# Performance work log

Measured on AMD Instinct MI355X. Metric: run time of the kernel, lower is better.

## Reference

```python
import jax, jax.numpy as jnp
import numpy as np

EMBED_DIM = 1024
NUM_HEADS = 16
HEAD_DIM = EMBED_DIM // NUM_HEADS
HIDDEN_DIM = int(EMBED_DIM * 4.0)
LN_EPS = 1e-5


def layer_norm(x, g, b):
    mu = jnp.mean(x, axis=-1, keepdims=True)
    var = jnp.var(x, axis=-1, keepdims=True)
    return (x - mu) * jax.lax.rsqrt(var + LN_EPS) * g + b


def setup_inputs() -> dict:
    key = jax.random.key(0)
    ks = jax.random.split(key, 8)
    D, H3, Dh = EMBED_DIM, 3 * EMBED_DIM, HIDDEN_DIM
    s = lambda fan: 1.0 / np.sqrt(fan)
    return {
        "x": jax.random.normal(ks[0], (2, 2048, D), dtype=jnp.float32),
        "ln1_g": jnp.ones((D,), jnp.float32),
        "ln1_b": jnp.zeros((D,), jnp.float32),
        "ln2_g": jnp.ones((D,), jnp.float32),
        "ln2_b": jnp.zeros((D,), jnp.float32),
        "w_qkv": jax.random.normal(ks[1], (D, H3), jnp.float32) * s(D),
        "b_qkv": jnp.zeros((H3,), jnp.float32),
        "w_proj": jax.random.normal(ks[2], (D, D), jnp.float32) * s(D),
        "b_proj": jnp.zeros((D,), jnp.float32),
        "w_fc1": jax.random.normal(ks[3], (D, Dh), jnp.float32) * s(D),
        "b_fc1": jnp.zeros((Dh,), jnp.float32),
        "w_fc2": jax.random.normal(ks[4], (Dh, D), jnp.float32) * s(Dh),
        "b_fc2": jnp.zeros((D,), jnp.float32),
    }


def reference(x, ln1_g, ln1_b, ln2_g, ln2_b, w_qkv, b_qkv, w_proj, b_proj,
              w_fc1, b_fc1, w_fc2, b_fc2):
    B, N, D = x.shape
    H, hd = NUM_HEADS, HEAD_DIM

    # --- attention branch (dropout inactive at eval) ---
    h = layer_norm(x, ln1_g, ln1_b)
    qkv = h @ w_qkv + b_qkv                      # [B,N,3D]
    qkv = qkv.reshape(B, N, 3, H, hd)
    q = qkv[:, :, 0].transpose(0, 2, 1, 3)       # [B,H,N,hd]
    k = qkv[:, :, 1].transpose(0, 2, 1, 3)
    v = qkv[:, :, 2].transpose(0, 2, 1, 3)
    scores = jnp.einsum('bhqd,bhkd->bhqk', q, k) / jnp.sqrt(jnp.float32(hd))
    attn = jax.nn.softmax(scores, axis=-1)
    ctx = jnp.einsum('bhqk,bhkd->bhqd', attn, v) # [B,H,N,hd]
    ctx = ctx.transpose(0, 2, 1, 3).reshape(B, N, D)
    x = x + ctx @ w_proj + b_proj

    # --- MLP branch ---
    h2 = layer_norm(x, ln2_g, ln2_b)
    h2 = jax.nn.gelu(h2 @ w_fc1 + b_fc1, approximate=False)  # torch nn.GELU = exact erf
    x = x + h2 @ w_fc2 + b_fc2
    return x
```

## Files before the change

### kernel.cpp

```cpp
#include <hip/hip_runtime.h>
#include <hip/hip_bf16.h>
#include <cstdint>

typedef __attribute__((ext_vector_type(8))) short short8;
typedef __attribute__((ext_vector_type(4))) float f32x4;

__device__ __forceinline__ uint16_t f2b(float f) {
  uint32_t u = __builtin_bit_cast(uint32_t, f);
  return (uint16_t)((u + 0x7FFFu + ((u >> 16) & 1u)) >> 16);
}
__device__ __forceinline__ float b2f(uint16_t h) {
  uint32_t u = ((uint32_t)h) << 16;
  return __builtin_bit_cast(float, u);
}
__device__ __forceinline__ void async16(void* lds, const void* g) {
  __builtin_amdgcn_global_load_lds(
      (const __attribute__((address_space(1))) uint32_t*)g,
      (__attribute__((address_space(3))) uint32_t*)lds, 16, 0, 0);
}
__device__ __forceinline__ void xcd_remap(int& bx, int& by, int& bz) {
  int gx = gridDim.x, gy = gridDim.y;
  int nwg = gx * gy * gridDim.z;
  int hw = blockIdx.x + gx * (blockIdx.y + gy * blockIdx.z);
  int work = ((nwg & 7) == 0) ? ((hw & 7) * (nwg >> 3) + (hw >> 3)) : hw;
  bx = work % gx;
  int t = work / gx;
  by = t % gy;
  bz = t / gy;
}

__global__ __launch_bounds__(256) void k_transpose_all(
    const float* __restrict__ wq, const float* __restrict__ wp,
    const float* __restrict__ w1, const float* __restrict__ w2,
    uint16_t* __restrict__ tq, uint16_t* __restrict__ tp,
    uint16_t* __restrict__ t1, uint16_t* __restrict__ t2) {
  __shared__ float tile[64][65];
  int id = blockIdx.x;
  const float* w; uint16_t* wT; int K, N, bx, by;
  if (id < 768)        { w = wq; wT = tq; K = 1024; N = 3072; bx = id % 48; by = id / 48; }
  else if (id < 1024)  { id -= 768;  w = wp; wT = tp; K = 1024; N = 1024; bx = id & 15; by = id >> 4; }
  else if (id < 2048)  { id -= 1024; w = w1; wT = t1; K = 1024; N = 4096; bx = id & 63; by = id >> 6; }
  else                 { id -= 2048; w = w2; wT = t2; K = 4096; N = 1024; bx = id & 15; by = id >> 4; }
  const int tx = threadIdx.x;
  const int k0 = by * 64, n0 = bx * 64;
  const int cr = tx & 15, rbase = tx >> 4;
#pragma unroll
  for (int rr = 0; rr < 4; ++rr) {
    int k = rbase + rr * 16;
    int n = cr * 4;
    float4 v = *(const float4*)&w[(size_t)(k0 + k) * N + (n0 + n)];
    tile[k][n + 0] = v.x; tile[k][n + 1] = v.y;
    tile[k][n + 2] = v.z; tile[k][n + 3] = v.w;
  }
  __syncthreads();
#pragma unroll
  for (int rr = 0; rr < 4; ++rr) {
    int n = rbase + rr * 16;
    int k = cr * 4;
    ushort4 o;
    o.x = f2b(tile[k + 0][n]);
    o.y = f2b(tile[k + 1][n]);
    o.z = f2b(tile[k + 2][n]);
    o.w = f2b(tile[k + 3][n]);
    *(ushort4*)&wT[(size_t)(n0 + n) * K + (k0 + k)] = o;
  }
}

__global__ __launch_bounds__(256) void k_layernorm(
    const float* __restrict__ x, const float* __restrict__ g,
    const float* __restrict__ b, uint16_t* __restrict__ out) {
  const int row = blockIdx.x * 4 + (threadIdx.x >> 6);
  const int lane = threadIdx.x & 63;
  const float* xr = x + (size_t)row * 1024;
  float4 v[4];
  float s = 0.f, ss = 0.f;
#pragma unroll
  for (int i = 0; i < 4; ++i) {
    v[i] = *(const float4*)&xr[i * 256 + lane * 4];
    s += v[i].x + v[i].y + v[i].z + v[i].w;
    ss += v[i].x * v[i].x + v[i].y * v[i].y + v[i].z * v[i].z + v[i].w * v[i].w;
  }
#pragma unroll
  for (int off = 1; off < 64; off <<= 1) {
    s += __shfl_xor(s, off);
    ss += __shfl_xor(ss, off);
  }
  float mu = s * (1.f / 1024.f);
  float rstd = rsqrtf(ss * (1.f / 1024.f) - mu * mu + 1e-5f);
#pragma unroll
  for (int i = 0; i < 4; ++i) {
    int col = i * 256 + lane * 4;
    float4 gv = *(const float4*)&g[col];
    float4 bv = *(const float4*)&b[col];
    ushort4 o;
    o.x = f2b((v[i].x - mu) * rstd * gv.x + bv.x);
    o.y = f2b((v[i].y - mu) * rstd * gv.y + bv.y);
    o.z = f2b((v[i].z - mu) * rstd * gv.z + bv.z);
    o.w = f2b((v[i].w - mu) * rstd * gv.w + bv.w);
    *(ushort4*)&out[(size_t)row * 1024 + col] = o;
  }
}

__global__ __launch_bounds__(256) void k_ln2_fuse(
    const float* __restrict__ x, const uint16_t* __restrict__ pp0,
    const uint16_t* __restrict__ pp1, const float* __restrict__ bias,
    const float* __restrict__ g, const float* __restrict__ b,
    float* __restrict__ x2, uint16_t* __restrict__ out) {
  const int row = blockIdx.x * 4 + (threadIdx.x >> 6);
  const int lane = threadIdx.x & 63;
  const size_t rb = (size_t)row * 1024;
  float4 v[4];
  float s = 0.f, ss = 0.f;
#pragma unroll
  for (int i = 0; i < 4; ++i) {
    int col = i * 256 + lane * 4;
    float4 xv = *(const float4*)&x[rb + col];
    float4 bv = *(const float4*)&bias[col];
    ushort4 a0 = *(const ushort4*)&pp0[rb + col];
    ushort4 a1 = *(const ushort4*)&pp1[rb + col];
    v[i].x = xv.x + bv.x + b2f(a0.x) + b2f(a1.x);
    v[i].y = xv.y + bv.y + b2f(a0.y) + b2f(a1.y);
    v[i].z = xv.z + bv.z + b2f(a0.z) + b2f(a1.z);
    v[i].w = xv.w + bv.w + b2f(a0.w) + b2f(a1.w);
    *(float4*)&x2[rb + col] = v[i];
    s += v[i].x + v[i].y + v[i].z + v[i].w;
    ss += v[i].x * v[i].x + v[i].y * v[i].y + v[i].z * v[i].z + v[i].w * v[i].w;
  }
#pragma unroll
  for (int off = 1; off < 64; off <<= 1) {
    s += __shfl_xor(s, off);
    ss += __shfl_xor(ss, off);
  }
  float mu = s * (1.f / 1024.f);
  float rstd = rsqrtf(ss * (1.f / 1024.f) - mu * mu + 1e-5f);
#pragma unroll
  for (int i = 0; i < 4; ++i) {
    int col = i * 256 + lane * 4;
    float4 gv = *(const float4*)&g[col];
    float4 bv = *(const float4*)&b[col];
    ushort4 o;
    o.x = f2b((v[i].x - mu) * rstd * gv.x + bv.x);
    o.y = f2b((v[i].y - mu) * rstd * gv.y + bv.y);
    o.z = f2b((v[i].z - mu) * rstd * gv.z + bv.z);
    o.w = f2b((v[i].w - mu) * rstd * gv.w + bv.w);
    *(ushort4*)&out[rb + col] = o;
  }
}

__global__ __launch_bounds__(256) void k_fc2_reduce(
    const float* __restrict__ x2, const uint16_t* __restrict__ f0,
    const uint16_t* __restrict__ f1, const float* __restrict__ bias,
    float* __restrict__ out, int N) {
  int i = (blockIdx.x * 256 + threadIdx.x) * 4;
  float4 v = *(const float4*)&x2[i];
  float4 bv = *(const float4*)&bias[i & (N - 1)];
  ushort4 a0 = *(const ushort4*)&f0[i];
  ushort4 a1 = *(const ushort4*)&f1[i];
  v.x += bv.x + b2f(a0.x) + b2f(a1.x);
  v.y += bv.y + b2f(a0.y) + b2f(a1.y);
  v.z += bv.z + b2f(a0.z) + b2f(a1.z);
  v.w += bv.w + b2f(a0.w) + b2f(a1.w);
  *(float4*)&out[i] = v;
}

template <int EPI>
__global__ __launch_bounds__(256) void k_gemm(
    const uint16_t* __restrict__ A, const uint16_t* __restrict__ Bt,
    const float* __restrict__ bias, void* __restrict__ Cout,
    uint16_t* __restrict__ vTout, int M, int N, int K) {
  __shared__ __align__(16) uint16_t Alds[128 * 64];
  __shared__ __align__(16) uint16_t Blds[128 * 64];
  int bx, by, bz;
  xcd_remap(bx, by, bz);
  const int tid = threadIdx.x;
  const int lane = tid & 63;
  const int w = tid >> 6;
  const int wr = w >> 1, wc = w & 1;
  const int m0 = by * 128, n0 = bx * 128;
  const int l15 = lane & 15, l4 = lane >> 4;
  const uint16_t* pA[4];
  const uint16_t* pB[4];
#pragma unroll
  for (int c = 0; c < 4; ++c) {
    int i = c * 256 + tid;
    int row = i >> 3, d = (i & 7) * 8;
    pA[c] = A + (size_t)(m0 + row) * K + d;
    pB[c] = Bt + (size_t)(n0 + row) * K + d;
  }
  f32x4 acc[4][4] = {};
  for (int k0 = 0; k0 < K; k0 += 64) {
#pragma unroll
    for (int c = 0; c < 4; ++c) {
      async16(&Alds[(c * 256 + tid) * 8], pA[c]);
      pA[c] += 64;
    }
#pragma unroll
    for (int c = 0; c < 4; ++c) {
      async16(&Blds[(c * 256 + tid) * 8], pB[c]);
      pB[c] += 64;
    }
    __syncthreads();
#pragma unroll
    for (int kc = 0; kc < 2; ++kc) {
      short8 af[4], bf[4];
#pragma unroll
      for (int m = 0; m < 4; ++m)
        af[m] = *(const short8*)&Alds[(wr * 64 + m * 16 + l15) * 64 + kc * 32 + l4 * 8];
#pragma unroll
      for (int n = 0; n < 4; ++n)
        bf[n] = *(const short8*)&Blds[(wc * 64 + n * 16 + l15) * 64 + kc * 32 + l4 * 8];
#pragma unroll
      for (int m = 0; m < 4; ++m)
#pragma unroll
        for (int n = 0; n < 4; ++n)
          acc[m][n] = __builtin_amdgcn_mfma_f32_16x16x32_bf16(af[m], bf[n], acc[m][n], 0, 0, 0);
    }
    __syncthreads();
  }
#pragma unroll
  for (int m = 0; m < 4; ++m) {
#pragma unroll
    for (int n = 0; n < 4; ++n) {
      int col = n0 + wc * 64 + n * 16 + l15;
      int rowb = m0 + wr * 64 + m * 16 + l4 * 4;
      float bv = bias[col];
      if constexpr (EPI == 3) {
        if (col >= 2048) {
          int dtot = col - 2048;
          int hh = dtot >> 6, dd = dtot & 63;
          int bg = rowb >> 11, tl = rowb & 2047;
          ushort4 ov;
          ov.x = f2b(acc[m][n][0] + bv);
          ov.y = f2b(acc[m][n][1] + bv);
          ov.z = f2b(acc[m][n][2] + bv);
          ov.w = f2b(acc[m][n][3] + bv);
          *(ushort4*)&vTout[(((size_t)(bg * 16 + hh)) * 64 + dd) * 2048 + tl] = ov;
          continue;
        }
      }
#pragma unroll
      for (int r = 0; r < 4; ++r) {
        float val = acc[m][n][r] + bv;
        size_t idx = (size_t)(rowb + r) * N + col;
        if constexpr (EPI == 2) {
          float u = val * val;
          float a = fmaf(u, 0.1029480545f, 2.3022078158f);
          float t = exp2f(val * a);
          float gl = val - val / (t + 1.0f);
          ((uint16_t*)Cout)[idx] = f2b(gl);
        } else {
          ((uint16_t*)Cout)[idx] = f2b(val);
        }
      }
    }
  }
}

__global__ __launch_bounds__(256) void k_gemm_splitk(
    const uint16_t* __restrict__ A, const uint16_t* __restrict__ Bt,
    uint16_t* __restrict__ p0, uint16_t* __restrict__ p1,
    int M, int N, int K, int Kc) {
  __shared__ __align__(16) uint16_t Alds[128 * 64];
  __shared__ __align__(16) uint16_t Blds[128 * 64];
  int bx, by, bz;
  xcd_remap(bx, by, bz);
  const int tid = threadIdx.x;
  const int lane = tid & 63;
  const int w = tid >> 6;
  const int wr = w >> 1, wc = w & 1;
  const int m0 = by * 128, n0 = bx * 128;
  const int l15 = lane & 15, l4 = lane >> 4;
  const int kbeg = bz * Kc;
  uint16_t* __restrict__ P = (bz == 0) ? p0 : p1;
  const uint16_t* pA[4];
  const uint16_t* pB[4];
#pragma unroll
  for (int c = 0; c < 4; ++c) {
    int i = c * 256 + tid;
    int row = i >> 3, d = (i & 7) * 8;
    pA[c] = A + (size_t)(m0 + row) * K + kbeg + d;
    pB[c] = Bt + (size_t)(n0 + row) * K + kbeg + d;
  }
  f32x4 acc[4][4] = {};
  for (int k0 = 0; k0 < Kc; k0 += 64) {
#pragma unroll
    for (int c = 0; c < 4; ++c) {
      async16(&Alds[(c * 256 + tid) * 8], pA[c]);
      pA[c] += 64;
    }
#pragma unroll
    for (int c = 0; c < 4; ++c) {
      async16(&Blds[(c * 256 + tid) * 8], pB[c]);
      pB[c] += 64;
    }
    __syncthreads();
#pragma unroll
    for (int kc = 0; kc < 2; ++kc) {
      short8 af[4], bf[4];
#pragma unroll
      for (int m = 0; m < 4; ++m)
        af[m] = *(const short8*)&Alds[(wr * 64 + m * 16 + l15) * 64 + kc * 32 + l4 * 8];
#pragma unroll
      for (int n = 0; n < 4; ++n)
        bf[n] = *(const short8*)&Blds[(wc * 64 + n * 16 + l15) * 64 + kc * 32 + l4 * 8];
#pragma unroll
      for (int m = 0; m < 4; ++m)
#pragma unroll
        for (int n = 0; n < 4; ++n)
          acc[m][n] = __builtin_amdgcn_mfma_f32_16x16x32_bf16(af[m], bf[n], acc[m][n], 0, 0, 0);
    }
    __syncthreads();
  }
#pragma unroll
  for (int m = 0; m < 4; ++m) {
#pragma unroll
    for (int n = 0; n < 4; ++n) {
      int col = n0 + wc * 64 + n * 16 + l15;
      int rowb = m0 + wr * 64 + m * 16 + l4 * 4;
#pragma unroll
      for (int r = 0; r < 4; ++r)
        P[(size_t)(rowb + r) * N + col] = f2b(acc[m][n][r]);
    }
  }
}

__global__ __launch_bounds__(256, 4) void k_attn(
    const uint16_t* __restrict__ qkv, const uint16_t* __restrict__ vT,
    uint16_t* __restrict__ ctx) {
  __shared__ __align__(16) uint16_t Klds[2][64 * 64];
  __shared__ __align__(16) uint16_t Vlds[2][64 * 64];
  __shared__ __align__(16) uint16_t Plds[4][16 * 64];
  int bx, by, bz;
  xcd_remap(bx, by, bz);
  const int bh = by, qt = bx;
  const int b = bh >> 4, h = bh & 15;
  const int tid = threadIdx.x, lane = tid & 63, w = tid >> 6;
  const int l15 = lane & 15, l4 = lane >> 4;
  const int sw = (l15 & 7) << 3;
  const size_t tokbase = (size_t)b * 2048;

  const float QSC = 0.125f * 1.44269504088896340736f;
  short8 qa[2];
  const int qrow = qt * 64 + w * 16 + l15;
#pragma unroll
  for (int kc = 0; kc < 2; ++kc) {
    short8 v = *(const short8*)&qkv[(tokbase + qrow) * 3072 + h * 64 + kc * 32 + l4 * 8];
#pragma unroll
    for (int j = 0; j < 8; ++j) v[j] = (short)f2b(b2f((uint16_t)v[j]) * QSC);
    qa[kc] = v;
  }
  short8 ones;
#pragma unroll
  for (int j = 0; j < 8; ++j) ones[j] = (short)0x3F80;

  float m_s = -1e30f;
  f32x4 o[4] = {};
  f32x4 ol = {};

  const uint16_t* pK[2];
  const uint16_t* pV[2];
#pragma unroll
  for (int c = 0; c < 2; ++c) {
    int i = c * 256 + tid;
    int row = i >> 3, colE = (i & 7) * 8;
    int colS = colE ^ ((row & 7) << 3);
    pK[c] = qkv + (tokbase + row) * 3072 + 1024 + h * 64 + colS;
    int tkS = colE ^ ((row & 7) << 3);
    pV[c] = vT + ((size_t)bh * 64 + row) * 2048 + tkS;
  }

  auto stage = [&](int buf) {
#pragma unroll
    for (int c = 0; c < 2; ++c) {
      async16(&Klds[buf][(c * 256 + tid) * 8], pK[c]);
      pK[c] += 64 * 3072;
    }
#pragma unroll
    for (int c = 0; c < 2; ++c) {
      async16(&Vlds[buf][(c * 256 + tid) * 8], pV[c]);
      pV[c] += 64;
    }
  };

  stage(0);
  __syncthreads();
  int cur = 0;

  for (int t0 = 0; t0 < 2048; t0 += 64) {
    if (t0 + 64 < 2048) stage(cur ^ 1);

    f32x4 s[4] = {};
    __builtin_amdgcn_s_setprio(1);
#pragma unroll
    for (int kc = 0; kc < 2; ++kc) {
      const int cc = (kc * 32 + l4 * 8) ^ sw;
#pragma unroll
      for (int c = 0; c < 4; ++c) {
        short8 kf = *(const short8*)&Klds[cur][(c * 16 + l15) * 64 + cc];
        s[c] = __builtin_amdgcn_mfma_f32_16x16x32_bf16(kf, qa[kc], s[c], 0, 0, 0);
      }
    }
    __builtin_amdgcn_s_setprio(0);

    {
      float a0 = fmaxf(fmaxf(s[0][0], s[0][1]), fmaxf(s[0][2], s[0][3]));
      float a1 = fmaxf(fmaxf(s[1][0], s[1][1]), fmaxf(s[1][2], s[1][3]));
      float a2 = fmaxf(fmaxf(s[2][0], s[2][1]), fmaxf(s[2][2], s[2][3]));
      float a3 = fmaxf(fmaxf(s[3][0], s[3][1]), fmaxf(s[3][2], s[3][3]));
      float pml = fmaxf(fmaxf(a0, a1), fmaxf(a2, a3));
      if (!__all(pml - m_s <= 8.f)) {
        float pm = pml;
        pm = fmaxf(pm, __shfl_xor(pm, 16));
        pm = fmaxf(pm, __shfl_xor(pm, 32));
        float mn = fmaxf(m_s, pm);
        float scale = exp2f(m_s - mn);
        m_s = mn;
        float sc0 = __shfl(scale, l4 * 4 + 0);
        float sc1 = __shfl(scale, l4 * 4 + 1);
        float sc2 = __shfl(scale, l4 * 4 + 2);
        float sc3 = __shfl(scale, l4 * 4 + 3);
#pragma unroll
        for (int df = 0; df < 4; ++df) {
          o[df][0] *= sc0; o[df][1] *= sc1; o[df][2] *= sc2; o[df][3] *= sc3;
        }
        ol[0] *= sc0; ol[1] *= sc1; ol[2] *= sc2; ol[3] *= sc3;
      }
#pragma unroll
      for (int c = 0; c < 4; ++c) {
        float p0 = exp2f(s[c][0] - m_s);
        float p1 = exp2f(s[c][1] - m_s);
        float p2 = exp2f(s[c][2] - m_s);
        float p3 = exp2f(s[c][3] - m_s);
        uint32_t lo, hi;
        asm("v_cvt_pk_bf16_f32 %0, %1, %2" : "=v"(lo) : "v"(p0), "v"(p1));
        asm("v_cvt_pk_bf16_f32 %0, %1, %2" : "=v"(hi) : "v"(p2), "v"(p3));
        *(uint2*)&Plds[w][l15 * 64 + ((c * 16 + l4 * 4) ^ sw)] = make_uint2(lo, hi);
      }
    }

    __builtin_amdgcn_s_setprio(1);
#pragma unroll
    for (int kc = 0; kc < 2; ++kc) {
      const int cc = (kc * 32 + l4 * 8) ^ sw;
      short8 pa = *(const short8*)&Plds[w][l15 * 64 + cc];
      ol = __builtin_amdgcn_mfma_f32_16x16x32_bf16(pa, ones, ol, 0, 0, 0);
#pragma unroll
      for (int df = 0; df < 4; ++df) {
        short8 vf = *(const short8*)&Vlds[cur][(df * 16 + l15) * 64 + cc];
        o[df] = __builtin_amdgcn_mfma_f32_16x16x32_bf16(pa, vf, o[df], 0, 0, 0);
      }
    }
    __builtin_amdgcn_s_setprio(0);
    __syncthreads();
    cur ^= 1;
  }

#pragma unroll
  for (int r = 0; r < 4; ++r) {
    float rl = 1.0f / ol[r];
    int tok = qt * 64 + w * 16 + l4 * 4 + r;
#pragma unroll
    for (int df = 0; df < 4; ++df) {
      ctx[(tokbase + tok) * 1024 + h * 64 + df * 16 + l15] = f2b(o[df][r] * rl);
    }
  }
}

extern "C" void kernel_launch(void* const* d_in, const int* in_sizes, int n_in,
                              void* d_out, int out_size, void* d_ws, size_t ws_size,
                              hipStream_t stream) {
  const float* x      = (const float*)d_in[0];
  const float* ln1_g  = (const float*)d_in[1];
  const float* ln1_b  = (const float*)d_in[2];
  const float* ln2_g  = (const float*)d_in[3];
  const float* ln2_b  = (const float*)d_in[4];
  const float* w_qkv  = (const float*)d_in[5];
  const float* b_qkv  = (const float*)d_in[6];
  const float* w_proj = (const float*)d_in[7];
  const float* b_proj = (const float*)d_in[8];
  const float* w_fc1  = (const float*)d_in[9];
  const float* b_fc1  = (const float*)d_in[10];
  const float* w_fc2  = (const float*)d_in[11];
  const float* b_fc2  = (const float*)d_in[12];
  float* out = (float*)d_out;
  char* ws = (char*)d_ws;
  const size_t MB = 1 << 20;

  uint16_t* wTfc1  = (uint16_t*)(ws + 0 * MB);
  uint16_t* wTfc2  = (uint16_t*)(ws + 8 * MB);
  uint16_t* wTqkv  = (uint16_t*)(ws + 16 * MB);
  uint16_t* wTproj = (uint16_t*)(ws + 22 * MB);
  uint16_t* hbuf   = (uint16_t*)(ws + 24 * MB);
  uint16_t* qkvb   = (uint16_t*)(ws + 32 * MB);
  uint16_t* vTb    = (uint16_t*)(ws + 56 * MB);
  uint16_t* ctxb   = (uint16_t*)(ws + 64 * MB);
  float*    x2b    = (float*)   (ws + 72 * MB);
  uint16_t* pp0    = (uint16_t*)(ws + 32 * MB);
  uint16_t* pp1    = (uint16_t*)(ws + 40 * MB);
  uint16_t* actb   = (uint16_t*)(ws + 32 * MB);
  uint16_t* fp0    = (uint16_t*)(ws + 16 * MB);
  uint16_t* fp1    = (uint16_t*)(ws + 24 * MB);

  k_transpose_all<<<3072, 256, 0, stream>>>(w_qkv, w_proj, w_fc1, w_fc2,
                                            wTqkv, wTproj, wTfc1, wTfc2);

  k_layernorm<<<1024, 256, 0, stream>>>(x, ln1_g, ln1_b, hbuf);
  k_gemm<3><<<dim3(24, 32), 256, 0, stream>>>(hbuf, wTqkv, b_qkv, qkvb, vTb, 4096, 3072, 1024);
  k_attn<<<dim3(32, 32), 256, 0, stream>>>(qkvb, vTb, ctxb);

  k_gemm_splitk<<<dim3(8, 32, 2), 256, 0, stream>>>(ctxb, wTproj, pp0, pp1,
                                                    4096, 1024, 1024, 512);
  k_ln2_fuse<<<1024, 256, 0, stream>>>(x, pp0, pp1, b_proj, ln2_g, ln2_b, x2b, hbuf);

  k_gemm<2><<<dim3(32, 32), 256, 0, stream>>>(hbuf, wTfc1, b_fc1, actb, nullptr, 4096, 4096, 1024);

  k_gemm_splitk<<<dim3(8, 32, 2), 256, 0, stream>>>(actb, wTfc2, fp0, fp1,
                                                    4096, 1024, 4096, 2048);
  k_fc2_reduce<<<4096, 256, 0, stream>>>(x2b, fp0, fp1, b_fc2, out, 1024);
}
```

Baseline: 293.5 us.

## Rewrite attention kernel with 32x32 MFMA and register-resident P

The attention kernel moves from 16x16x32 MFMA tiles with 4 waves of 16 query rows to 32x32x16 MFMA tiles with 2 waves of 32 query rows each. Softmax probabilities are packed to bf16 and rearranged in registers with permlane32 swaps, so they feed the PV MFMA directly instead of going through an LDS round trip. The row sum is now kept as a scalar accumulated on the VALU rather than computed by an extra MFMA against a ones vector. The aim is to cut LDS traffic and MFMA issue overhead, at the cost of 128-thread blocks, higher register pressure per wave and possibly lower occupancy.

```diff
diff --git a/kernel.cpp b/kernel.cpp
--- a/kernel.cpp
+++ b/kernel.cpp
@@ -4,6 +4,7 @@
 
 typedef __attribute__((ext_vector_type(8))) short short8;
 typedef __attribute__((ext_vector_type(4))) float f32x4;
+typedef __attribute__((ext_vector_type(16))) float f32x16;
 
 __device__ __forceinline__ uint16_t f2b(float f) {
   uint32_t u = __builtin_bit_cast(uint32_t, f);
@@ -324,60 +325,52 @@
   }
 }
 
-__global__ __launch_bounds__(256, 4) void k_attn(
+__global__ __launch_bounds__(128) void k_attn(
     const uint16_t* __restrict__ qkv, const uint16_t* __restrict__ vT,
     uint16_t* __restrict__ ctx) {
   __shared__ __align__(16) uint16_t Klds[2][64 * 64];
   __shared__ __align__(16) uint16_t Vlds[2][64 * 64];
-  __shared__ __align__(16) uint16_t Plds[4][16 * 64];
   int bx, by, bz;
   xcd_remap(bx, by, bz);
   const int bh = by, qt = bx;
-  const int b = bh >> 4, h = bh & 15;
-  const int tid = threadIdx.x, lane = tid & 63, w = tid >> 6;
-  const int l15 = lane & 15, l4 = lane >> 4;
-  const int sw = (l15 & 7) << 3;
+  const int b = bh >> 4, hh = bh & 15;
+  const int tid = threadIdx.x, lane = tid & 63, wv = tid >> 6;
+  const int l31 = lane & 31, hf = lane >> 5;
+  const int swz = (lane & 7) << 3;
   const size_t tokbase = (size_t)b * 2048;
 
   const float QSC = 0.125f * 1.44269504088896340736f;
-  short8 qa[2];
-  const int qrow = qt * 64 + w * 16 + l15;
-#pragma unroll
-  for (int kc = 0; kc < 2; ++kc) {
-    short8 v = *(const short8*)&qkv[(tokbase + qrow) * 3072 + h * 64 + kc * 32 + l4 * 8];
+  short8 qb[4];
+  const int qrow = qt * 64 + wv * 32 + l31;
+#pragma unroll
+  for (int ks = 0; ks < 4; ++ks) {
+    short8 v = *(const short8*)&qkv[(tokbase + qrow) * 3072 + hh * 64 + ks * 16 + hf * 8];
 #pragma unroll
     for (int j = 0; j < 8; ++j) v[j] = (short)f2b(b2f((uint16_t)v[j]) * QSC);
-    qa[kc] = v;
-  }
-  short8 ones;
-#pragma unroll
-  for (int j = 0; j < 8; ++j) ones[j] = (short)0x3F80;
-
-  float m_s = -1e30f;
-  f32x4 o[4] = {};
-  f32x4 ol = {};
-
-  const uint16_t* pK[2];
-  const uint16_t* pV[2];
-#pragma unroll
-  for (int c = 0; c < 2; ++c) {
-    int i = c * 256 + tid;
-    int row = i >> 3, colE = (i & 7) * 8;
-    int colS = colE ^ ((row & 7) << 3);
-    pK[c] = qkv + (tokbase + row) * 3072 + 1024 + h * 64 + colS;
-    int tkS = colE ^ ((row & 7) << 3);
-    pV[c] = vT + ((size_t)bh * 64 + row) * 2048 + tkS;
-  }
-
+    qb[ks] = v;
+  }
+
+  float m_s = -1e30f, ls = 0.f;
+  f32x16 o0 = {}, o1 = {};
+
+  const uint16_t* pK[4];
+  const uint16_t* pV[4];
+#pragma unroll
+  for (int c = 0; c < 4; ++c) {
+    int row = c * 16 + (tid >> 3);
+    int colS = ((tid & 7) * 8) ^ ((row & 7) << 3);
+    pK[c] = qkv + (tokbase + row) * 3072 + 1024 + hh * 64 + colS;
+    pV[c] = vT + ((size_t)bh * 64 + row) * 2048 + colS;
+  }
   auto stage = [&](int buf) {
 #pragma unroll
-    for (int c = 0; c < 2; ++c) {
-      async16(&Klds[buf][(c * 256 + tid) * 8], pK[c]);
+    for (int c = 0; c < 4; ++c) {
+      async16(&Klds[buf][(c * 128 + tid) * 8], pK[c]);
       pK[c] += 64 * 3072;
     }
 #pragma unroll
-    for (int c = 0; c < 2; ++c) {
-      async16(&Vlds[buf][(c * 256 + tid) * 8], pV[c]);
+    for (int c = 0; c < 4; ++c) {
+      async16(&Vlds[buf][(c * 128 + tid) * 8], pV[c]);
       pV[c] += 64;
     }
   };
@@ -389,80 +382,87 @@
   for (int t0 = 0; t0 < 2048; t0 += 64) {
     if (t0 + 64 < 2048) stage(cur ^ 1);
 
-    f32x4 s[4] = {};
+    f32x16 s0 = {}, s1 = {};
     __builtin_amdgcn_s_setprio(1);
 #pragma unroll
-    for (int kc = 0; kc < 2; ++kc) {
-      const int cc = (kc * 32 + l4 * 8) ^ sw;
-#pragma unroll
-      for (int c = 0; c < 4; ++c) {
-        short8 kf = *(const short8*)&Klds[cur][(c * 16 + l15) * 64 + cc];
-        s[c] = __builtin_amdgcn_mfma_f32_16x16x32_bf16(kf, qa[kc], s[c], 0, 0, 0);
-      }
+    for (int ks = 0; ks < 4; ++ks) {
+      const int cc = (ks * 16 + hf * 8) ^ swz;
+      short8 kf0 = *(const short8*)&Klds[cur][l31 * 64 + cc];
+      short8 kf1 = *(const short8*)&Klds[cur][(32 + l31) * 64 + cc];
+      s0 = __builtin_amdgcn_mfma_f32_32x32x16_bf16(kf0, qb[ks], s0, 0, 0, 0);
+      s1 = __builtin_amdgcn_mfma_f32_32x32x16_bf16(kf1, qb[ks], s1, 0, 0, 0);
     }
     __builtin_amdgcn_s_setprio(0);
 
-    {
-      float a0 = fmaxf(fmaxf(s[0][0], s[0][1]), fmaxf(s[0][2], s[0][3]));
-      float a1 = fmaxf(fmaxf(s[1][0], s[1][1]), fmaxf(s[1][2], s[1][3]));
-      float a2 = fmaxf(fmaxf(s[2][0], s[2][1]), fmaxf(s[2][2], s[2][3]));
-      float a3 = fmaxf(fmaxf(s[3][0], s[3][1]), fmaxf(s[3][2], s[3][3]));
-      float pml = fmaxf(fmaxf(a0, a1), fmaxf(a2, a3));
-      if (!__all(pml - m_s <= 8.f)) {
-        float pm = pml;
-        pm = fmaxf(pm, __shfl_xor(pm, 16));
-        pm = fmaxf(pm, __shfl_xor(pm, 32));
-        float mn = fmaxf(m_s, pm);
-        float scale = exp2f(m_s - mn);
-        m_s = mn;
-        float sc0 = __shfl(scale, l4 * 4 + 0);
-        float sc1 = __shfl(scale, l4 * 4 + 1);
-        float sc2 = __shfl(scale, l4 * 4 + 2);
-        float sc3 = __shfl(scale, l4 * 4 + 3);
-#pragma unroll
-        for (int df = 0; df < 4; ++df) {
-          o[df][0] *= sc0; o[df][1] *= sc1; o[df][2] *= sc2; o[df][3] *= sc3;
-        }
-        ol[0] *= sc0; ol[1] *= sc1; ol[2] *= sc2; ol[3] *= sc3;
-      }
-#pragma unroll
-      for (int c = 0; c < 4; ++c) {
-        float p0 = exp2f(s[c][0] - m_s);
-        float p1 = exp2f(s[c][1] - m_s);
-        float p2 = exp2f(s[c][2] - m_s);
-        float p3 = exp2f(s[c][3] - m_s);
-        uint32_t lo, hi;
-        asm("v_cvt_pk_bf16_f32 %0, %1, %2" : "=v"(lo) : "v"(p0), "v"(p1));
-        asm("v_cvt_pk_bf16_f32 %0, %1, %2" : "=v"(hi) : "v"(p2), "v"(p3));
-        *(uint2*)&Plds[w][l15 * 64 + ((c * 16 + l4 * 4) ^ sw)] = make_uint2(lo, hi);
-      }
+    float pml = fmaxf(s0[0], s1[0]);
+#pragma unroll
+    for (int r = 1; r < 16; ++r) pml = fmaxf(pml, fmaxf(s0[r], s1[r]));
+    if (!__all(pml - m_s <= 8.f)) {
+      float pm = fmaxf(pml, __shfl_xor(pml, 32));
+      float mn = fmaxf(m_s, pm);
+      float sc = exp2f(m_s - mn);
+      m_s = mn;
+      ls *= sc;
+      o0 *= sc;
+      o1 *= sc;
+    }
+
+    short8 pf[4];
+#pragma unroll
+    for (int kb = 0; kb < 2; ++kb) {
+      float p[16];
+#pragma unroll
+      for (int r = 0; r < 16; ++r) p[r] = exp2f(((kb == 0) ? s0[r] : s1[r]) - m_s);
+      ls += (((p[0] + p[1]) + (p[2] + p[3])) + ((p[4] + p[5]) + (p[6] + p[7]))) +
+            (((p[8] + p[9]) + (p[10] + p[11])) + ((p[12] + p[13]) + (p[14] + p[15])));
+      uint32_t A0, B0, C0, D0, A1, B1, C1, D1;
+      asm("v_cvt_pk_bf16_f32 %0, %1, %2" : "=v"(A0) : "v"(p[0]), "v"(p[1]));
+      asm("v_cvt_pk_bf16_f32 %0, %1, %2" : "=v"(B0) : "v"(p[2]), "v"(p[3]));
+      asm("v_cvt_pk_bf16_f32 %0, %1, %2" : "=v"(C0) : "v"(p[4]), "v"(p[5]));
+      asm("v_cvt_pk_bf16_f32 %0, %1, %2" : "=v"(D0) : "v"(p[6]), "v"(p[7]));
+      asm("v_cvt_pk_bf16_f32 %0, %1, %2" : "=v"(A1) : "v"(p[8]), "v"(p[9]));
+      asm("v_cvt_pk_bf16_f32 %0, %1, %2" : "=v"(B1) : "v"(p[10]), "v"(p[11]));
+      asm("v_cvt_pk_bf16_f32 %0, %1, %2" : "=v"(C1) : "v"(p[12]), "v"(p[13]));
+      asm("v_cvt_pk_bf16_f32 %0, %1, %2" : "=v"(D1) : "v"(p[14]), "v"(p[15]));
+      asm("v_permlane32_swap_b32 %0, %1" : "+v"(A0), "+v"(C0));
+      asm("v_permlane32_swap_b32 %0, %1" : "+v"(B0), "+v"(D0));
+      asm("v_permlane32_swap_b32 %0, %1" : "+v"(A1), "+v"(C1));
+      asm("v_permlane32_swap_b32 %0, %1" : "+v"(B1), "+v"(D1));
+      pf[kb * 2 + 0] = __builtin_bit_cast(short8, make_uint4(A0, B0, C0, D0));
+      pf[kb * 2 + 1] = __builtin_bit_cast(short8, make_uint4(A1, B1, C1, D1));
     }
 
     __builtin_amdgcn_s_setprio(1);
 #pragma unroll
-    for (int kc = 0; kc < 2; ++kc) {
-      const int cc = (kc * 32 + l4 * 8) ^ sw;
-      short8 pa = *(const short8*)&Plds[w][l15 * 64 + cc];
-      ol = __builtin_amdgcn_mfma_f32_16x16x32_bf16(pa, ones, ol, 0, 0, 0);
-#pragma unroll
-      for (int df = 0; df < 4; ++df) {
-        short8 vf = *(const short8*)&Vlds[cur][(df * 16 + l15) * 64 + cc];
-        o[df] = __builtin_amdgcn_mfma_f32_16x16x32_bf16(pa, vf, o[df], 0, 0, 0);
-      }
+    for (int t = 0; t < 4; ++t) {
+      const int cc = (t * 16 + hf * 8) ^ swz;
+      short8 vf0 = *(const short8*)&Vlds[cur][l31 * 64 + cc];
+      short8 vf1 = *(const short8*)&Vlds[cur][(32 + l31) * 64 + cc];
+      o0 = __builtin_amdgcn_mfma_f32_32x32x16_bf16(vf0, pf[t], o0, 0, 0, 0);
+      o1 = __builtin_amdgcn_mfma_f32_32x32x16_bf16(vf1, pf[t], o1, 0, 0, 0);
     }
     __builtin_amdgcn_s_setprio(0);
     __syncthreads();
     cur ^= 1;
   }
 
-#pragma unroll
-  for (int r = 0; r < 4; ++r) {
-    float rl = 1.0f / ol[r];
-    int tok = qt * 64 + w * 16 + l4 * 4 + r;
-#pragma unroll
-    for (int df = 0; df < 4; ++df) {
-      ctx[(tokbase + tok) * 1024 + h * 64 + df * 16 + l15] = f2b(o[df][r] * rl);
-    }
+  float lt = ls + __shfl_xor(ls, 32);
+  float rl = 1.0f / lt;
+  const size_t obase = (tokbase + qrow) * 1024 + hh * 64;
+#pragma unroll
+  for (int g = 0; g < 4; ++g) {
+    ushort4 ov;
+    ov.x = f2b(o0[g * 4 + 0] * rl);
+    ov.y = f2b(o0[g * 4 + 1] * rl);
+    ov.z = f2b(o0[g * 4 + 2] * rl);
+    ov.w = f2b(o0[g * 4 + 3] * rl);
+    *(ushort4*)&ctx[obase + g * 8 + hf * 4] = ov;
+    ushort4 ow;
+    ow.x = f2b(o1[g * 4 + 0] * rl);
+    ow.y = f2b(o1[g * 4 + 1] * rl);
+    ow.z = f2b(o1[g * 4 + 2] * rl);
+    ow.w = f2b(o1[g * 4 + 3] * rl);
+    *(ushort4*)&ctx[obase + 32 + g * 8 + hf * 4] = ow;
   }
 }
 
@@ -506,7 +506,7 @@
 
   k_layernorm<<<1024, 256, 0, stream>>>(x, ln1_g, ln1_b, hbuf);
   k_gemm<3><<<dim3(24, 32), 256, 0, stream>>>(hbuf, wTqkv, b_qkv, qkvb, vTb, 4096, 3072, 1024);
-  k_attn<<<dim3(32, 32), 256, 0, stream>>>(qkvb, vTb, ctxb);
+  k_attn<<<dim3(32, 32), 128, 0, stream>>>(qkvb, vTb, ctxb);
 
   k_gemm_splitk<<<dim3(8, 32, 2), 256, 0, stream>>>(ctxb, wTproj, pp0, pp1,
                                                     4096, 1024, 1024, 512);
```

New measurement: 304.5 us. 3.8% more time.
